# Kernel optimization log

Hardware: AMD Instinct MI355X
Metric: run time of the kernel (lower is better)

Reference implementation:

```python
import jax, jax.numpy as jnp
import numpy as np

B, S, DIM = 2, 1024, 1024
N_EXPERTS, K = 8, 2
VOCAB = 16384
HIDDEN = DIM * 8 // 3          # 2730
UP_OUT = HIDDEN * 2            # 5460 (swiglu doubling)


def setup_inputs() -> dict:
    key = jax.random.key(0)
    ks = jax.random.split(key, 5)
    x = jax.random.normal(ks[0], (B, S, DIM), dtype=jnp.float32)
    w_router = jax.random.normal(ks[1], (N_EXPERTS, DIM), dtype=jnp.float32) * 0.02
    w_up = jax.random.normal(ks[2], (N_EXPERTS, UP_OUT, DIM), dtype=jnp.float32) * 0.02
    w_down = jax.random.normal(ks[3], (N_EXPERTS, DIM, HIDDEN), dtype=jnp.float32) * 0.02
    w_proj = jax.random.normal(ks[4], (N_EXPERTS, VOCAB, DIM), dtype=jnp.float32) * 0.02
    return {"x": x, "w_router": w_router, "w_up": w_up, "w_down": w_down, "w_proj": w_proj}


def _grouped_linear(x_sorted, weight, group_sizes):
    # weight: [n_experts, out, in] (torch Linear layout) -> ragged_dot wants [g, in, out]
    return jax.lax.ragged_dot(x_sorted, jnp.swapaxes(weight, 1, 2), group_sizes)


def reference(x, w_router, w_up, w_down, w_proj):
    b, s, d = x.shape
    # Router (eval path): plain top-k of linear scores
    scores = jnp.einsum("bsd,nd->bsn", x, w_router)
    c, ids = jax.lax.top_k(scores, K)                   # [B,S,K]
    # Dispatch: replicate tokens k times, sort by expert id (stable, matching torch.sort)
    xe = jnp.broadcast_to(x[..., None, :], (b, s, K, d)).reshape(-1, d)   # [T, d]
    ids_flat = ids.reshape(-1)
    order = jnp.argsort(ids_flat)                        # stable sort indices
    x_sorted = xe[order]
    group_sizes = jnp.bincount(ids_flat, length=N_EXPERTS).astype(jnp.int32)
    # Expert swiglu MLP with residual (grouped GEMMs)
    skip = x_sorted
    h = _grouped_linear(x_sorted, w_up, group_sizes)     # [T, 2*HIDDEN]
    h_lin, h_gate = jnp.split(h, 2, axis=-1)
    h = h_lin * jax.nn.silu(h_gate)
    h = _grouped_linear(h, w_down, group_sizes) + skip   # [T, d]
    logits = _grouped_linear(h, w_proj, group_sizes)     # [T, VOCAB]
    # Postprocess: scatter back to original token order
    out = jnp.zeros_like(logits).at[order].set(logits)
    out = out.reshape(b, s, K, VOCAB)
    # Weighted top-k combine
    w = jax.nn.softmax(c, axis=-1)                       # [B,S,K]
    return jnp.sum(out * w[..., None], axis=-2)          # [B,S,VOCAB]
```

## Files before the change

kernel.cpp:

```cpp
#include <hip/hip_runtime.h>
#include <hip/hip_bf16.h>

typedef __bf16 bf16_t;
typedef __bf16 bf16x2 __attribute__((ext_vector_type(2)));
typedef __bf16 bf16x4 __attribute__((ext_vector_type(4)));
typedef __bf16 bf16x8 __attribute__((ext_vector_type(8)));
typedef float f32x4 __attribute__((ext_vector_type(4)));

#define DIM     1024
#define NEXP    8
#define VOCAB   16384
#define HIDDEN  2730
#define UPOUT   5460
#define NTOK    2048
#define NSLOT   4096
#define HRAW_LD 5472
#define H1_LD   2752
#define BM      256
#define MAXTILES 24

#define WS_COUNTS      0
#define WS_NTILES      64
#define WS_TILE_E      128
#define WS_TILE_M0     256
#define WS_TILE_MEND   384
#define WS_SLOT_IDS    1024
#define WS_SLOT_W      20480
#define WS_SLOT_OF_POS 40960
#define WS_POS_OF_SLOT 61440
#define WS_XSORTED     131072
#define WS_H2          8519680
#define WS_H1          16908288
#define WS_HRAW        39452672
#define WS_LOGITS      16908288ull
#define WS_NEED_BIG    (WS_LOGITS + (size_t)NSLOT * VOCAB * 2)

__device__ __forceinline__ void gload_lds16(const void* g, void* l) {
    __builtin_amdgcn_global_load_lds((const __attribute__((address_space(1))) void*)g,
                                     (__attribute__((address_space(3))) void*)l, 16, 0, 0);
}
__device__ __forceinline__ int swzm(int r) { return (r ^ (r >> 2)) & 3; }

__global__ __launch_bounds__(256) void router_kernel(const float* __restrict__ x,
        const float* __restrict__ wr, int* __restrict__ slot_ids,
        float* __restrict__ slot_w, int* __restrict__ counts) {
    const int lane = threadIdx.x & 63;
    const int wave = threadIdx.x >> 6;
    const int token = blockIdx.x * 4 + wave;
    const float* xrow = x + (size_t)token * DIM;
    float acc[NEXP];
#pragma unroll
    for (int e = 0; e < NEXP; ++e) acc[e] = 0.f;
#pragma unroll
    for (int i = 0; i < DIM / 64; ++i) {
        const int k = i * 64 + lane;
        const float xv = xrow[k];
#pragma unroll
        for (int e = 0; e < NEXP; ++e) acc[e] += xv * wr[e * DIM + k];
    }
#pragma unroll
    for (int off = 32; off > 0; off >>= 1) {
#pragma unroll
        for (int e = 0; e < NEXP; ++e) acc[e] += __shfl_xor(acc[e], off);
    }
    if (lane == 0) {
        float c0 = -1e30f; int b0 = 0;
#pragma unroll
        for (int e = 0; e < NEXP; ++e) if (acc[e] > c0) { c0 = acc[e]; b0 = e; }
        float c1 = -1e30f; int b1 = 0;
#pragma unroll
        for (int e = 0; e < NEXP; ++e) if (e != b0 && acc[e] > c1) { c1 = acc[e]; b1 = e; }
        slot_ids[token * 2 + 0] = b0;
        slot_ids[token * 2 + 1] = b1;
        const float w0 = 1.f / (1.f + expf(c1 - c0));
        slot_w[token * 2 + 0] = w0;
        slot_w[token * 2 + 1] = 1.f - w0;
        atomicAdd(&counts[b0], 1);
        atomicAdd(&counts[b1], 1);
    }
}

__global__ __launch_bounds__(512) void sched_kernel(const int* __restrict__ counts,
        int* __restrict__ ntiles, int* __restrict__ tile_e, int* __restrict__ tile_m0,
        int* __restrict__ tile_mend, const int* __restrict__ slot_ids,
        int* __restrict__ slot_of_pos, int* __restrict__ pos_of_slot) {
    __shared__ int offs[NEXP];
    if (threadIdx.x == 0) {
        int o = 0, nt = 0;
        for (int e = 0; e < NEXP; ++e) {
            offs[e] = o;
            const int c = counts[e];
            for (int m = 0; m < c; m += BM) {
                tile_e[nt] = e; tile_m0[nt] = o + m; tile_mend[nt] = o + c; ++nt;
            }
            o += c;
        }
        *ntiles = nt;
    }
    __syncthreads();
    const int e = threadIdx.x >> 6;
    const int lane = threadIdx.x & 63;
    int base = offs[e];
    for (int ch = 0; ch < NSLOT / 64; ++ch) {
        const int i = ch * 64 + lane;
        const int id = slot_ids[i];
        const unsigned long long m = __ballot(id == e);
        if (id == e) {
            const int rank = __popcll(m & ((1ull << lane) - 1ull));
            slot_of_pos[base + rank] = i;
            pos_of_slot[i] = base + rank;
        }
        base += __popcll(m);
    }
}

__global__ __launch_bounds__(256) void gather_kernel(const float* __restrict__ x,
        const int* __restrict__ slot_of_pos, bf16_t* __restrict__ xs) {
    const int row = blockIdx.x;
    const int t = threadIdx.x;
    const int tok = slot_of_pos[row] >> 1;
    const float4 v = *(const float4*)(x + (size_t)tok * DIM + t * 4);
    bf16x4 o;
    o.x = (bf16_t)v.x; o.y = (bf16_t)v.y; o.z = (bf16_t)v.z; o.w = (bf16_t)v.w;
    *(bf16x4*)(xs + (size_t)row * DIM + t * 4) = o;
}

__global__ __launch_bounds__(256) void swiglu_kernel(const bf16_t* __restrict__ hraw,
        bf16_t* __restrict__ h1) {
    const int row = blockIdx.x;
    const int col = blockIdx.y * 256 + threadIdx.x;
    if (col >= H1_LD) return;
    float o = 0.f;
    if (col < HIDDEN) {
        const float a = (float)hraw[(size_t)row * HRAW_LD + col];
        const float g = (float)hraw[(size_t)row * HRAW_LD + col + HIDDEN];
        o = a * (g / (1.f + expf(-g)));
    }
    h1[(size_t)row * H1_LD + col] = (bf16_t)o;
}

__global__ __launch_bounds__(256) void combine_kernel(const bf16_t* __restrict__ logits,
        const int* __restrict__ pos_of_slot, const float* __restrict__ slot_w,
        float* __restrict__ out) {
    const int t = blockIdx.x;
    const int v0 = (blockIdx.y * 256 + threadIdx.x) * 8;
    const int p0 = pos_of_slot[2 * t], p1 = pos_of_slot[2 * t + 1];
    const float w0 = slot_w[2 * t], w1 = slot_w[2 * t + 1];
    const bf16x8 a = *(const bf16x8*)(logits + (size_t)p0 * VOCAB + v0);
    const bf16x8 b = *(const bf16x8*)(logits + (size_t)p1 * VOCAB + v0);
    float o[8];
#pragma unroll
    for (int i = 0; i < 8; ++i) o[i] = w0 * (float)a[i] + w1 * (float)b[i];
    *(float4*)(out + (size_t)t * VOCAB + v0)     = make_float4(o[0], o[1], o[2], o[3]);
    *(float4*)(out + (size_t)t * VOCAB + v0 + 4) = make_float4(o[4], o[5], o[6], o[7]);
}

template <int EPI, bool SWZ>
__global__ __launch_bounds__(1024, 4) void gemm_pk(
        const bf16_t* __restrict__ A,
        const float* __restrict__ B, int N,
        bf16_t* __restrict__ C, int ldc,
        const int* __restrict__ slot_of_pos,
        const float* __restrict__ slot_w,
        float* __restrict__ outp,
        const int* __restrict__ tile_e,
        const int* __restrict__ tile_m0,
        const int* __restrict__ tile_mend,
        const int* __restrict__ ntiles) {
    if (blockIdx.y >= (unsigned)*ntiles) return;
    constexpr int K = 1024, KT = 32;
    int bx = blockIdx.x;
    if constexpr (SWZ) bx = (bx & 7) * (gridDim.x >> 3) + (bx >> 3);
    const int e = tile_e[blockIdx.y];
    const int m0 = tile_m0[blockIdx.y];
    const int mend = tile_mend[blockIdx.y];
    const int n0 = bx * 256;
    const float* __restrict__ Bexp = B + (size_t)e * N * K;

    __shared__ bf16_t sA[2][128][64];
    __shared__ bf16_t sB[2][128][64];

    const int tid = threadIdx.x;
    const int lane = tid & 63;
    const int wave = tid >> 6;
    const int wr = wave >> 2;
    const int wc = wave & 3;
    const int fr = lane & 15;
    const int fq = lane >> 4;

    const int a_ou = (lane & 7) ^ (lane >> 3);
    const int a_r  = wave * 8 + (lane >> 3) + ((a_ou & 4) << 5);
    const int a_k16 = (a_ou & 3) * 8;

    const int bp  = tid >> 3;
    const int bu  = tid & 7;
    const int bou = bu ^ (bp & 7);
    const int b_row = bp + ((bou & 4) << 5);
    const int b_k   = (bou & 3) * 8;
    const float* bsrc = Bexp + (size_t)min(n0 + b_row, N - 1) * K + b_k;

    f32x4 acc[4][4] = {};

    auto stageA = [&](int buf, int kt) {
        const int k0 = min(kt, KT - 1) * 32;
        const int gr = min(m0 + a_r, NSLOT - 1);
        gload_lds16(A + (size_t)gr * K + k0 + a_k16, &sA[buf][wave * 8][0]);
    };
    auto loadB = [&](int kt, f32x4& v0, f32x4& v1) {
        const int k0 = min(kt, KT - 1) * 32;
        v0 = *(const f32x4*)(bsrc + k0);
        v1 = *(const f32x4*)(bsrc + k0 + 4);
    };
    auto writeB = [&](int buf, const f32x4& v0, const f32x4& v1) {
        bf16x8 t;
        t[0] = (bf16_t)v0[0]; t[1] = (bf16_t)v0[1];
        t[2] = (bf16_t)v0[2]; t[3] = (bf16_t)v0[3];
        t[4] = (bf16_t)v1[0]; t[5] = (bf16_t)v1[1];
        t[6] = (bf16_t)v1[2]; t[7] = (bf16_t)v1[3];
        *(bf16x8*)&sB[buf][bp][bu * 8] = t;
    };
    auto compute = [&](int buf) {
        bf16x8 bb[4];
#pragma unroll
        for (int ni = 0; ni < 4; ++ni) {
            const int r = wc * 64 + ni * 16 + fr;
            const int p = r & 127;
            const int u = (((r >> 7) << 2) + fq) ^ (fr & 7);
            bb[ni] = *(const bf16x8*)&sB[buf][p][u * 8];
        }
        __builtin_amdgcn_s_setprio(1);
#pragma unroll
        for (int mi = 0; mi < 4; ++mi) {
            const int r = wr * 64 + mi * 16 + fr;
            const int p = r & 127;
            const int u = (((r >> 7) << 2) + fq) ^ (fr & 7);
            const bf16x8 af = *(const bf16x8*)&sA[buf][p][u * 8];
#pragma unroll
            for (int ni = 0; ni < 4; ++ni)
                acc[mi][ni] = __builtin_amdgcn_mfma_f32_16x16x32_bf16(
                        af, bb[ni], acc[mi][ni], 0, 0, 0);
        }
        __builtin_amdgcn_s_setprio(0);
    };

    f32x4 P0, P1, Q0, Q1;
    loadB(0, P0, P1);
    stageA(0, 0);
    loadB(1, Q0, Q1);
    asm volatile("s_waitcnt vmcnt(3)" ::: "memory");
    writeB(0, P0, P1);
    asm volatile("s_waitcnt lgkmcnt(0)" ::: "memory");
    stageA(1, 1);

    for (int kt = 0; kt < KT; kt += 2) {
        loadB(kt + 2, P0, P1);
        asm volatile("s_waitcnt vmcnt(3)" ::: "memory");
        __builtin_amdgcn_s_barrier();
        asm volatile("" ::: "memory");
        writeB(1, Q0, Q1);
        compute(0);
        asm volatile("s_waitcnt lgkmcnt(0)" ::: "memory");
        __builtin_amdgcn_s_barrier();
        asm volatile("" ::: "memory");
        stageA(0, kt + 2);
        loadB(kt + 3, Q0, Q1);
        asm volatile("s_waitcnt vmcnt(3)" ::: "memory");
        __builtin_amdgcn_s_barrier();
        asm volatile("" ::: "memory");
        writeB(0, P0, P1);
        compute(1);
        asm volatile("s_waitcnt lgkmcnt(0)" ::: "memory");
        __builtin_amdgcn_s_barrier();
        asm volatile("" ::: "memory");
        stageA(1, kt + 3);
    }

#pragma unroll
    for (int mi = 0; mi < 4; ++mi) {
#pragma unroll
        for (int reg = 0; reg < 4; ++reg) {
            const int r = m0 + wr * 64 + mi * 16 + fq * 4 + reg;
            if (r >= mend) continue;
            int tok = 0; float wgt = 0.f;
            if constexpr (EPI == 2) {
                const int slot = slot_of_pos[r];
                tok = slot >> 1;
                wgt = slot_w[slot];
            }
#pragma unroll
            for (int ni = 0; ni < 4; ++ni) {
                const int c = n0 + wc * 64 + ni * 16 + fr;
                if (c >= N) continue;
                float v = acc[mi][ni][reg];
                if constexpr (EPI == 0) {
                    C[(size_t)r * ldc + c] = (bf16_t)v;
                } else {
                    unsafeAtomicAdd(&outp[(size_t)tok * VOCAB + c], v * wgt);
                }
            }
        }
    }
}

template <int EPI, int BN, bool SWZ>
__global__ __launch_bounds__(1024, 4) void gemm_mid(
        const bf16_t* __restrict__ A, int lda,
        const float* __restrict__ B, int N, int K, int KT, long bLast,
        bf16_t* __restrict__ C, int ldc,
        const bf16_t* __restrict__ skip,
        const int* __restrict__ tile_e,
        const int* __restrict__ tile_m0,
        const int* __restrict__ tile_mend,
        const int* __restrict__ ntiles) {
    if (blockIdx.y >= (unsigned)*ntiles) return;
    int bx = blockIdx.x;
    if constexpr (SWZ) bx = (bx & 7) * (gridDim.x >> 3) + (bx >> 3);
    const int e = tile_e[blockIdx.y];
    const int m0 = tile_m0[blockIdx.y];
    const int mend = tile_mend[blockIdx.y];
    const int n0 = bx * BN;

    constexpr int NI = BN / 64;

    __shared__ bf16_t sA[2][BM][32];
    __shared__ bf16_t sB[2][BN][32];

    const int tid = threadIdx.x;
    const int lane = tid & 63;
    const int wave = tid >> 6;
    const int wr = wave >> 2;
    const int wc = wave & 3;
    const int fr = lane & 15;
    const int fq = lane >> 4;

    f32x4 acc[4][NI] = {};

    auto stageA = [&](int buf, int kt) {
        const int k0 = min(kt, KT - 1) * 32;
        const int rb = wave * 16;
        const int r = rb + (lane >> 2);
        const int gr = min(m0 + r, NSLOT - 1);
        const int c16 = (lane & 3) ^ swzm(r);
        gload_lds16(A + (size_t)gr * lda + k0 + c16 * 8, &sA[buf][rb][0]);
    };
    auto loadB = [&](int kt, float2& vc) {
        const int k0 = min(kt, KT - 1) * 32;
        long fl = (long)e * N * K + (long)(n0 + wave * 4 + (lane >> 4)) * K
                  + k0 + (lane & 15) * 2;
        if (fl > bLast) fl = bLast;
        vc = *(const float2*)(B + fl);
    };
    auto writeB = [&](int buf, const float2& vc) {
        const int r = wave * 4 + (lane >> 4);
        bf16x2 t; t.x = (bf16_t)vc.x; t.y = (bf16_t)vc.y;
        const int q = lane & 15;
        char* p = (char*)&sB[buf][r][0] + (((q >> 2) ^ swzm(r)) * 16) + (q & 3) * 4;
        *(bf16x2*)p = t;
    };
    auto compute = [&](int buf) {
        bf16x8 af[4], bb[NI];
#pragma unroll
        for (int mi = 0; mi < 4; ++mi) {
            const int r = wr * 64 + mi * 16 + fr;
            af[mi] = *(const bf16x8*)&sA[buf][r][(fq ^ swzm(r)) * 8];
        }
#pragma unroll
        for (int ni = 0; ni < NI; ++ni) {
            const int r = wc * (BN / 4) + ni * 16 + fr;
            bb[ni] = *(const bf16x8*)&sB[buf][r][(fq ^ swzm(r)) * 8];
        }
        __builtin_amdgcn_s_setprio(1);
#pragma unroll
        for (int ni = 0; ni < NI; ++ni)
#pragma unroll
            for (int mi = 0; mi < 4; ++mi)
                acc[mi][ni] = __builtin_amdgcn_mfma_f32_16x16x32_bf16(
                        af[mi], bb[ni], acc[mi][ni], 0, 0, 0);
        __builtin_amdgcn_s_setprio(0);
    };

    float2 Pc, Qc;
    loadB(0, Pc);
    stageA(0, 0);
    loadB(1, Qc);
    asm volatile("s_waitcnt vmcnt(2)" ::: "memory");
    writeB(0, Pc);
    asm volatile("s_waitcnt lgkmcnt(0)" ::: "memory");
    stageA(1, 1);

    for (int kt = 0; kt < KT; kt += 2) {
        loadB(kt + 2, Pc);
        asm volatile("s_waitcnt vmcnt(2)" ::: "memory");
        __builtin_amdgcn_s_barrier();
        asm volatile("" ::: "memory");
        writeB(1, Qc);
        compute(0);
        asm volatile("s_waitcnt lgkmcnt(0)" ::: "memory");
        __builtin_amdgcn_s_barrier();
        asm volatile("" ::: "memory");
        stageA(0, kt + 2);
        loadB(kt + 3, Qc);
        asm volatile("s_waitcnt vmcnt(2)" ::: "memory");
        __builtin_amdgcn_s_barrier();
        asm volatile("" ::: "memory");
        writeB(0, Pc);
        compute(1);
        asm volatile("s_waitcnt lgkmcnt(0)" ::: "memory");
        __builtin_amdgcn_s_barrier();
        asm volatile("" ::: "memory");
        stageA(1, kt + 3);
    }

#pragma unroll
    for (int mi = 0; mi < 4; ++mi) {
#pragma unroll
        for (int reg = 0; reg < 4; ++reg) {
            const int r = m0 + wr * 64 + mi * 16 + fq * 4 + reg;
            if (r >= mend) continue;
#pragma unroll
            for (int ni = 0; ni < NI; ++ni) {
                const int c = n0 + wc * (BN / 4) + ni * 16 + fr;
                if (c >= N) continue;
                float v = acc[mi][ni][reg];
                if constexpr (EPI == 1) v += (float)skip[(size_t)r * DIM + c];
                C[(size_t)r * ldc + c] = (bf16_t)v;
            }
        }
    }
}

extern "C" void kernel_launch(void* const* d_in, const int* in_sizes, int n_in,
                              void* d_out, int out_size, void* d_ws, size_t ws_size,
                              hipStream_t stream) {
    const float* x        = (const float*)d_in[0];
    const float* w_router = (const float*)d_in[1];
    const float* w_up     = (const float*)d_in[2];
    const float* w_down   = (const float*)d_in[3];
    const float* w_proj   = (const float*)d_in[4];
    float* out = (float*)d_out;
    char* ws = (char*)d_ws;

    int*    counts      = (int*)(ws + WS_COUNTS);
    int*    ntiles      = (int*)(ws + WS_NTILES);
    int*    tile_e      = (int*)(ws + WS_TILE_E);
    int*    tile_m0     = (int*)(ws + WS_TILE_M0);
    int*    tile_mend   = (int*)(ws + WS_TILE_MEND);
    int*    slot_ids    = (int*)(ws + WS_SLOT_IDS);
    float*  slot_w      = (float*)(ws + WS_SLOT_W);
    int*    slot_of_pos = (int*)(ws + WS_SLOT_OF_POS);
    int*    pos_of_slot = (int*)(ws + WS_POS_OF_SLOT);
    bf16_t* x_sorted    = (bf16_t*)(ws + WS_XSORTED);
    bf16_t* h2          = (bf16_t*)(ws + WS_H2);
    bf16_t* h1          = (bf16_t*)(ws + WS_H1);
    bf16_t* h_raw       = (bf16_t*)(ws + WS_HRAW);
    bf16_t* logits      = (bf16_t*)(ws + WS_LOGITS);

    const bool bigws = ws_size >= WS_NEED_BIG;

    hipMemsetAsync(d_ws, 0, 1024, stream);

    router_kernel<<<NTOK / 4, 256, 0, stream>>>(x, w_router, slot_ids, slot_w, counts);
    sched_kernel<<<1, 512, 0, stream>>>(counts, ntiles, tile_e, tile_m0, tile_mend,
                                        slot_ids, slot_of_pos, pos_of_slot);
    gather_kernel<<<NSLOT, 256, 0, stream>>>(x, slot_of_pos, x_sorted);

    gemm_pk<0, false><<<dim3((UPOUT + 255) / 256, MAXTILES), 1024, 0, stream>>>(
        x_sorted, w_up, UPOUT, h_raw, HRAW_LD,
        nullptr, nullptr, nullptr, tile_e, tile_m0, tile_mend, ntiles);

    swiglu_kernel<<<dim3(NSLOT, (H1_LD + 255) / 256), 256, 0, stream>>>(h_raw, h1);

    gemm_mid<1, 64, true><<<dim3(DIM / 64, MAXTILES), 1024, 0, stream>>>(
        h1, H1_LD, w_down, DIM, HIDDEN, (HIDDEN + 31) / 32,
        (long)NEXP * DIM * HIDDEN - 2,
        h2, DIM, x_sorted, tile_e, tile_m0, tile_mend, ntiles);

    if (bigws) {
        gemm_pk<0, true><<<dim3(VOCAB / 256, MAXTILES), 1024, 0, stream>>>(
            h2, w_proj, VOCAB, logits, VOCAB,
            nullptr, nullptr, nullptr, tile_e, tile_m0, tile_mend, ntiles);
        combine_kernel<<<dim3(NTOK, VOCAB / (256 * 8)), 256, 0, stream>>>(
            logits, pos_of_slot, slot_w, out);
    } else {
        hipMemsetAsync(d_out, 0, (size_t)out_size * sizeof(float), stream);
        gemm_pk<2, true><<<dim3(VOCAB / 256, MAXTILES), 1024, 0, stream>>>(
            h2, w_proj, VOCAB, nullptr, 0,
            slot_of_pos, slot_w, out, tile_e, tile_m0, tile_mend, ntiles);
    }
}
```

Measured before the change: 648.3 us.

## Deepen GEMM software pipeline with triple-buffered A and four-stage B prefetch

Restructures the K-loop of the grouped GEMM kernel into a deeper pipeline. A tiles are triple-buffered in LDS and B fp32 loads are prefetched four steps ahead in registers. Each step now needs one barrier instead of two, cutting synchronisation and exposing more global-load latency hiding. The cost is more LDS and more registers for the extra B prefetch, which may lower occupancy, and the vmcnt accounting must be exact to stay correct.

```diff
diff --git a/kernel.cpp b/kernel.cpp
--- a/kernel.cpp
+++ b/kernel.cpp
@@ -177,7 +177,7 @@
     const int n0 = bx * 256;
     const float* __restrict__ Bexp = B + (size_t)e * N * K;
 
-    __shared__ bf16_t sA[2][128][64];
+    __shared__ bf16_t sA[3][128][64];
     __shared__ bf16_t sB[2][128][64];
 
     const int tid = threadIdx.x;
@@ -219,14 +219,14 @@
         t[6] = (bf16_t)v1[2]; t[7] = (bf16_t)v1[3];
         *(bf16x8*)&sB[buf][bp][bu * 8] = t;
     };
-    auto compute = [&](int buf) {
+    auto compute = [&](int bufA, int bufB) {
         bf16x8 bb[4];
 #pragma unroll
         for (int ni = 0; ni < 4; ++ni) {
             const int r = wc * 64 + ni * 16 + fr;
             const int p = r & 127;
             const int u = (((r >> 7) << 2) + fq) ^ (fr & 7);
-            bb[ni] = *(const bf16x8*)&sB[buf][p][u * 8];
+            bb[ni] = *(const bf16x8*)&sB[bufB][p][u * 8];
         }
         __builtin_amdgcn_s_setprio(1);
 #pragma unroll
@@ -234,7 +234,7 @@
             const int r = wr * 64 + mi * 16 + fr;
             const int p = r & 127;
             const int u = (((r >> 7) << 2) + fq) ^ (fr & 7);
-            const bf16x8 af = *(const bf16x8*)&sA[buf][p][u * 8];
+            const bf16x8 af = *(const bf16x8*)&sA[bufA][p][u * 8];
 #pragma unroll
             for (int ni = 0; ni < 4; ++ni)
                 acc[mi][ni] = __builtin_amdgcn_mfma_f32_16x16x32_bf16(
@@ -243,36 +243,34 @@
         __builtin_amdgcn_s_setprio(0);
     };
 
-    f32x4 P0, P1, Q0, Q1;
-    loadB(0, P0, P1);
-    stageA(0, 0);
-    loadB(1, Q0, Q1);
-    asm volatile("s_waitcnt vmcnt(3)" ::: "memory");
-    writeB(0, P0, P1);
-    asm volatile("s_waitcnt lgkmcnt(0)" ::: "memory");
-    stageA(1, 1);
-
-    for (int kt = 0; kt < KT; kt += 2) {
-        loadB(kt + 2, P0, P1);
-        asm volatile("s_waitcnt vmcnt(3)" ::: "memory");
-        __builtin_amdgcn_s_barrier();
-        asm volatile("" ::: "memory");
-        writeB(1, Q0, Q1);
-        compute(0);
+    auto step = [&](int t, f32x4& Wa, f32x4& Wb,
+                    f32x4& La, f32x4& Lb) {
+        asm volatile("s_waitcnt vmcnt(5)" ::: "memory");
         asm volatile("s_waitcnt lgkmcnt(0)" ::: "memory");
         __builtin_amdgcn_s_barrier();
         asm volatile("" ::: "memory");
-        stageA(0, kt + 2);
-        loadB(kt + 3, Q0, Q1);
-        asm volatile("s_waitcnt vmcnt(3)" ::: "memory");
-        __builtin_amdgcn_s_barrier();
-        asm volatile("" ::: "memory");
-        writeB(0, P0, P1);
-        compute(1);
-        asm volatile("s_waitcnt lgkmcnt(0)" ::: "memory");
-        __builtin_amdgcn_s_barrier();
-        asm volatile("" ::: "memory");
-        stageA(1, kt + 3);
+        stageA((t + 2) % 3, t + 2);
+        loadB(t + 4, La, Lb);
+        writeB((t + 1) & 1, Wa, Wb);
+        compute(t % 3, t & 1);
+        asm volatile("" ::: "memory");
+    };
+
+    f32x4 R0a, R0b, R1a, R1b, R2a, R2b, R3a, R3b;
+    loadB(0, R0a, R0b);
+    loadB(1, R1a, R1b);
+    stageA(0, 0);
+    loadB(2, R2a, R2b);
+    stageA(1, 1);
+    loadB(3, R3a, R3b);
+    asm volatile("s_waitcnt vmcnt(8)" ::: "memory");
+    writeB(0, R0a, R0b);
+
+    for (int t = 0; t < KT; t += 4) {
+        step(t + 0, R1a, R1b, R0a, R0b);
+        step(t + 1, R2a, R2b, R1a, R1b);
+        step(t + 2, R3a, R3b, R2a, R2b);
+        step(t + 3, R0a, R0b, R3a, R3b);
     }
 
 #pragma unroll
```

Result: slower. 693.3 us (+6.9%).
